# Optimization experiments

Measured on AMD Instinct MI355X. Metric: run time of the kernel, lower is better.

The kernel has to match this reference:

```python
import jax, jax.numpy as jnp
import numpy as np

N_HEADS = 16


def setup_inputs() -> dict:
    key = jax.random.key(0)
    ks = jax.random.split(key, 5)
    B, T, C = 4, 2048, 1024
    return {
        "x": jax.random.normal(ks[0], (B, T, C), dtype=jnp.float32),
        "W_qkv": jax.random.normal(ks[1], (C, 3 * C), dtype=jnp.float32) * 0.02,
        "b_qkv": jax.random.normal(ks[2], (3 * C,), dtype=jnp.float32) * 0.02,
        "W_proj": jax.random.normal(ks[3], (C, C), dtype=jnp.float32) * 0.02,
        "b_proj": jax.random.normal(ks[4], (C,), dtype=jnp.float32) * 0.02,
    }


def reference(x, W_qkv, b_qkv, W_proj, b_proj):
    B, T, C = x.shape
    H = N_HEADS
    hs = C // H
    # QKV projection. NOTE: original reshapes (B,T,3C) -> (B,T,H,3*hs) then
    # chunks last dim, so q/k/v are interleaved per-head slices of the output.
    qkv = x @ W_qkv + b_qkv                       # [B, T, 3C]
    qkv = qkv.reshape(B, T, H, 3 * hs).transpose(0, 2, 1, 3)  # [B, H, T, 3*hs]
    q, k, v = jnp.split(qkv, 3, axis=-1)          # each [B, H, T, hs]
    scale = 1.0 / (hs ** 0.5)
    scores = jnp.einsum("bhqd,bhkd->bhqk", q, k) * scale  # [B, H, T, T]
    causal = jnp.tril(jnp.ones((T, T), dtype=bool))
    scores = jnp.where(causal, scores, jnp.float32(-1e9))
    attn = jax.nn.softmax(scores, axis=-1)
    out = jnp.einsum("bhqk,bhkd->bhqd", attn, v)  # [B, H, T, hs]
    out = out.transpose(0, 2, 1, 3).reshape(B, T, C)
    return out @ W_proj + b_proj
```

## Files before the change

kernel.cpp:

```cpp
#include <hip/hip_runtime.h>

typedef unsigned short u16;
typedef unsigned int u32;
typedef __attribute__((ext_vector_type(8))) short short8;
typedef __attribute__((ext_vector_type(8))) unsigned short u16x8;
typedef __attribute__((ext_vector_type(4))) unsigned short u16x4;
typedef __attribute__((ext_vector_type(2))) unsigned int u32x2;
typedef __attribute__((ext_vector_type(4))) float f32x4;

__device__ __forceinline__ u16 f2bf(float f){
  u32 u = __builtin_bit_cast(u32, f);
  u32 r = u + 0x7FFFu + ((u >> 16) & 1u);
  return (u16)(r >> 16);
}
__device__ __forceinline__ float bf2f(u16 h){
  u32 u = ((u32)h) << 16;
  return __builtin_bit_cast(float, u);
}
__device__ __forceinline__ u32 cvtpk(float lo, float hi){
  u32 r;
  asm("v_cvt_pk_bf16_f32 %0, %1, %2" : "=v"(r) : "v"(lo), "v"(hi));
  return r;
}
__device__ __forceinline__ float fexp2(float x){
  float r;
  asm("v_exp_f32 %0, %1" : "=v"(r) : "v"(x));
  return r;
}

__device__ __forceinline__ void gld_lds16(const u16* g, u16* l){
  __builtin_amdgcn_global_load_lds(
      (const __attribute__((address_space(1))) u32*)g,
      (__attribute__((address_space(3))) u32*)l, 16, 0, 0);
}

#define MFMA(a,b,c) __builtin_amdgcn_mfma_f32_16x16x32_bf16((a),(b),(c),0,0,0)

__global__ __launch_bounds__(256) void k_prep(const float* __restrict__ x,
                                              u16* __restrict__ xb,
                                              const float* __restrict__ Wqkv,
                                              u16* __restrict__ wqkvT,
                                              const float* __restrict__ Wproj,
                                              u16* __restrict__ wprojT){
  __shared__ float tile[32][33];
  int bid = blockIdx.x, tid = threadIdx.x;
  if (bid < 4096){
    int i = bid*256 + tid;
    const float4 a = ((const float4*)x)[2*i];
    const float4 b = ((const float4*)x)[2*i+1];
    u16x8 o;
    o[0]=f2bf(a.x); o[1]=f2bf(a.y); o[2]=f2bf(a.z); o[3]=f2bf(a.w);
    o[4]=f2bf(b.x); o[5]=f2bf(b.y); o[6]=f2bf(b.z); o[7]=f2bf(b.w);
    ((u16x8*)xb)[i] = o;
    return;
  }
  const float* in; u16* out; int R, C, bx, by;
  if (bid < 7168){
    int b2 = bid - 4096;
    in = Wqkv; out = wqkvT; R = 1024; C = 3072;
    bx = b2 % 96; by = b2 / 96;
  } else {
    int b3 = bid - 7168;
    in = Wproj; out = wprojT; R = 1024; C = 1024;
    bx = b3 % 32; by = b3 / 32;
  }
  int c0 = bx*32, r0 = by*32;
  int tx = tid & 31, ty = tid >> 5;
  #pragma unroll
  for (int i=0;i<4;i++) tile[ty+8*i][tx] = in[(size_t)(r0+ty+8*i)*C + c0+tx];
  __syncthreads();
  #pragma unroll
  for (int i=0;i<4;i++) out[(size_t)(c0+ty+8*i)*R + r0+tx] = f2bf(tile[tx][ty+8*i]);
}

#define GS_A(T_, BUF) do{                                                      \
  size_t k0_ = (size_t)(T_)*64;                                                \
  _Pragma("unroll")                                                            \
  for (int l=0;l<2;l++){                                                       \
    int r_ = l*64 + (tid>>3);                                                  \
    gld_lds16(Ag + (size_t)(brow + r_)*1024 + k0_ + (((tid&7)^(r_&7))*8),      \
              &Alds[(BUF)*8192 + l*4096 + tid*8]);                             \
  }                                                                            \
}while(0)

#define GS_B(T_, BUF, H_) do{                                                  \
  size_t k0_ = (size_t)(T_)*64;                                                \
  _Pragma("unroll")                                                            \
  for (int l=0;l<2;l++){                                                       \
    int r_ = (H_)*128 + l*64 + (tid>>3);                                       \
    gld_lds16(Bg + (size_t)(bcol + r_)*1024 + k0_ + (((tid&7)^(r_&7))*8),      \
              &Blds[(BUF)*16384 + (H_)*8192 + l*4096 + tid*8]);                \
  }                                                                            \
}while(0)

#define RD_A(MQ, CUR) do{                                                      \
  _Pragma("unroll")                                                            \
  for (int m=0;m<2;m++)                                                        \
    _Pragma("unroll")                                                          \
    for (int k=0;k<2;k++){                                                     \
      int hr = wr*64 + (MQ)*32 + m*16 + lr16;                                  \
      af[(MQ)*2+m][k] = *(const short8*)&Alds[(CUR)*8192 + hr*64 + (((k*4+lg)^(hr&7))*8)]; \
    }                                                                          \
}while(0)

#define RD_B(NQ, CUR) do{                                                      \
  _Pragma("unroll")                                                            \
  for (int n=0;n<2;n++)                                                        \
    _Pragma("unroll")                                                          \
    for (int k=0;k<2;k++){                                                     \
      int hr = wc*64 + (NQ)*32 + n*16 + lr16;                                  \
      bfv[(NQ)*2+n][k] = *(const short8*)&Blds[(CUR)*16384 + hr*64 + (((k*4+lg)^(hr&7))*8)]; \
    }                                                                          \
}while(0)

#define MF8(MQ, NQ)                                                            \
  _Pragma("unroll")                                                            \
  for (int k=0;k<2;k++)                                                        \
    _Pragma("unroll")                                                          \
    for (int m=0;m<2;m++)                                                      \
      _Pragma("unroll")                                                        \
      for (int n=0;n<2;n++)                                                    \
        acc[(MQ)*2+m][(NQ)*2+n] = MFMA(af[(MQ)*2+m][k], bfv[(NQ)*2+n][k], acc[(MQ)*2+m][(NQ)*2+n]);

#define G_TILE(T_, CUR, PF) do{                                                \
  RD_A(0, CUR); RD_B(0, CUR);                                                  \
  if (PF) GS_A((T_)+1, (CUR)^1);                                               \
  __builtin_amdgcn_s_barrier();                                                \
  __builtin_amdgcn_s_setprio(1); MF8(0,0); __builtin_amdgcn_s_setprio(0);      \
  __builtin_amdgcn_s_barrier();                                                \
  RD_B(1, CUR);                                                                \
  if (PF) GS_B((T_)+1, (CUR)^1, 0);                                            \
  __builtin_amdgcn_s_barrier();                                                \
  __builtin_amdgcn_s_setprio(1); MF8(0,1); __builtin_amdgcn_s_setprio(0);      \
  __builtin_amdgcn_s_barrier();                                                \
  RD_A(1, CUR);                                                                \
  if (PF) GS_B((T_)+1, (CUR)^1, 1);                                            \
  __builtin_amdgcn_s_barrier();                                                \
  __builtin_amdgcn_s_setprio(1); MF8(1,1); __builtin_amdgcn_s_setprio(0);      \
  __builtin_amdgcn_s_barrier();                                                \
  __builtin_amdgcn_s_setprio(1); MF8(1,0); __builtin_amdgcn_s_setprio(0);      \
  asm volatile("s_waitcnt vmcnt(0)" ::: "memory");                             \
  __builtin_amdgcn_sched_barrier(0);                                           \
  __builtin_amdgcn_s_barrier();                                                \
}while(0)

template<int OUT_BF16>
__global__ __launch_bounds__(512, 2) void gemm_ph(const u16* __restrict__ Ag,
                                                  const u16* __restrict__ Bg,
                                                  const float* __restrict__ bias,
                                                  void* __restrict__ Cp, int N){
  extern __shared__ u16 lds[];
  u16* Alds = lds;
  u16* Blds = lds + 16384;
  int tid = threadIdx.x, lane = tid&63, wid = tid>>6;
  int wr = wid>>2, wc = wid&3;
  int lr16 = lane&15, lg = lane>>4;
  int nbx = gridDim.x;
  int nwg = nbx*gridDim.y;
  int lin = blockIdx.y*nbx + blockIdx.x;
  int cpx = nwg>>3;
  int swz = (lin&7)*cpx + (lin>>3);
  int bx = swz % nbx, by = swz / nbx;
  size_t brow = (size_t)by*128, bcol = (size_t)bx*256;
  f32x4 acc[4][4] = {};
  short8 af[4][2], bfv[4][2];

  GS_A(0, 0);
  GS_B(0, 0, 0);
  GS_B(0, 0, 1);
  __syncthreads();

  #pragma unroll 1
  for (int kt=0; kt<16; kt+=2){
    G_TILE(kt,   0, true);
    G_TILE(kt+1, 1, (kt+2<16));
  }

  #pragma unroll
  for (int ni=0;ni<4;ni++){
    size_t col = bcol + wc*64 + ni*16 + lr16;
    float bs = bias[col];
    #pragma unroll
    for (int mi=0;mi<4;mi++)
      #pragma unroll
      for (int j=0;j<4;j++){
        size_t row = brow + wr*64 + mi*16 + lg*4 + j;
        float v = acc[mi][ni][j] + bs;
        if (OUT_BF16) ((u16*)Cp)[row*(size_t)N + col] = f2bf(v);
        else          ((float*)Cp)[row*(size_t)N + col] = v;
      }
  }
}

#define ATTN_ITER(KB, CUR, PF) do{                                             \
  int kv0 = (KB)*64;                                                           \
  if (PF){                                                                     \
    int kv1 = kv0 + 64;                                                        \
    va[0] = *(const u16x4*)(qkv + (bt0 + kv1 + vr0    )*3072 + hq + 128 + vd0);\
    va[1] = *(const u16x4*)(qkv + (bt0 + kv1 + vr0 + 1)*3072 + hq + 128 + vd0);\
    gld_lds16(qkv + (bt0+kv1+kr)*3072 + hq + 64 + kcs, &Ks[(CUR)^1][tid*8]);   \
  }                                                                            \
  f32x4 st[4];                                                                 \
  __builtin_amdgcn_s_setprio(1);                                               \
  _Pragma("unroll")                                                            \
  for (int s=0;s<4;s++){                                                       \
    short8 kf0 = *(const short8*)&Ks[CUR][(s*16+lr16)*64 + ((lg  )^rx)*8];     \
    short8 kf1 = *(const short8*)&Ks[CUR][(s*16+lr16)*64 + ((4+lg)^rx)*8];     \
    f32x4 z = {0,0,0,0};                                                       \
    z = MFMA(kf0, qf[0], z);                                                   \
    z = MFMA(kf1, qf[1], z);                                                   \
    st[s] = z;                                                                 \
  }                                                                            \
  __builtin_amdgcn_s_setprio(0);                                               \
  if (kv0 >= qbase){                                                           \
    _Pragma("unroll")                                                          \
    for (int s=0;s<4;s++)                                                      \
      _Pragma("unroll")                                                        \
      for (int j=0;j<4;j++){                                                   \
        int kvg = kv0 + s*16 + lg*4 + j;                                       \
        if (kvg > qglob) st[s][j] = -1e30f;                                    \
      }                                                                        \
  }                                                                            \
  {                                                                            \
    u32 pw[8];                                                                 \
    _Pragma("unroll")                                                          \
    for (int s=0;s<4;s++){                                                     \
      float p0 = fexp2(st[s][0]), p1 = fexp2(st[s][1]);                        \
      float p2 = fexp2(st[s][2]), p3 = fexp2(st[s][3]);                        \
      pw[s*2+0] = cvtpk(p0,p1);                                                \
      pw[s*2+1] = cvtpk(p2,p3);                                                \
    }                                                                          \
    _Pragma("unroll")                                                          \
    for (int s=0;s<4;s++){                                                     \
      int cp = (s*2 + (lg>>1)) ^ rx;                                           \
      u32x2 w2; w2[0] = pw[s*2]; w2[1] = pw[s*2+1];                            \
      *(u32x2*)&Pl[wv][lr16*64 + cp*8 + (lg&1)*4] = w2;                        \
    }                                                                          \
  }                                                                            \
  if (PF){                                                                     \
    _Pragma("unroll")                                                          \
    for (int k=0;k<4;k++){                                                     \
      int d = vd0+k;                                                           \
      int c = (vr0>>3) ^ (d&7) ^ ((d>>3)&7);                                   \
      u32 w = (u32)va[0][k] | ((u32)va[1][k]<<16);                             \
      *(u32*)&Vt[(CUR)^1][d*64 + c*8 + (vr0&7)] = w;                           \
    }                                                                          \
  }                                                                            \
  __builtin_amdgcn_s_setprio(1);                                               \
  _Pragma("unroll")                                                            \
  for (int B=0;B<2;B++){                                                       \
    short8 pa = *(const short8*)&Pl[wv][lr16*64 + (((B<<2)+lg)^rx)*8];         \
    acc_l = MFMA(pa, onesf, acc_l);                                            \
    _Pragma("unroll")                                                          \
    for (int db=0;db<4;db++){                                                  \
      int d = db*16 + lr16;                                                    \
      short8 vf = *(const short8*)&Vt[CUR][d*64 + ((((B<<2)+lg)^(d&7))^((d>>3)&7))*8]; \
      O[db] = MFMA(pa, vf, O[db]);                                             \
    }                                                                          \
  }                                                                            \
  __builtin_amdgcn_s_setprio(0);                                               \
  __syncthreads();                                                             \
}while(0)

__global__ __launch_bounds__(512, 4) void k_attn(const u16* __restrict__ qkv,
                                                 u16* __restrict__ o, int T){
  __shared__ __align__(16) u16 Ks[2][64*64];
  __shared__ __align__(16) u16 Vt[2][64*64];
  __shared__ __align__(16) u16 Pl[8][16*64];
  int tid = threadIdx.x, lane = tid&63, wv = tid>>6;
  int bh = blockIdx.x;
  int b = bh>>4, h = bh&15;
  int hq = h*192;
  size_t bt0 = (size_t)b*T;
  int lr16 = lane&15, lg = lane>>4;
  int rx = lr16&7;
  int vr0 = (tid>>4)*2, vd0 = (tid&15)*4;
  int kr  = tid>>3;
  int kcs = ((tid&7) ^ (kr&7))*8;
  u16x4 va[2];
  const float QS = 0.18033688f;
  u16x8 ov;
  #pragma unroll
  for (int j=0;j<8;j++) ov[j] = 0x3F80;
  const short8 onesf = __builtin_bit_cast(short8, ov);

  #pragma unroll 1
  for (int half=0; half<2; ++half){
    int qt = half ? (int)blockIdx.y : 15 - (int)blockIdx.y;
    int qbase = qt*128;
    short8 qf[2];
    {
      const u16* qp = qkv + (bt0 + qbase + wv*16 + lr16)*3072 + hq + lg*8;
      #pragma unroll
      for (int t=0;t<2;t++){
        u16x8 v = *(const u16x8*)(qp + t*32);
        #pragma unroll
        for (int j=0;j<8;j++) v[j] = f2bf(bf2f(v[j])*QS);
        qf[t] = __builtin_bit_cast(short8, v);
      }
    }
    f32x4 O[4] = {};
    f32x4 acc_l = {0,0,0,0};
    int qglob = qbase + wv*16 + lr16;

    {
      va[0] = *(const u16x4*)(qkv + (bt0 + vr0    )*3072 + hq + 128 + vd0);
      va[1] = *(const u16x4*)(qkv + (bt0 + vr0 + 1)*3072 + hq + 128 + vd0);
      gld_lds16(qkv + (bt0+kr)*3072 + hq + 64 + kcs, &Ks[0][tid*8]);
      #pragma unroll
      for (int k=0;k<4;k++){
        int d = vd0+k;
        int c = (vr0>>3) ^ (d&7) ^ ((d>>3)&7);
        u32 w = (u32)va[0][k] | ((u32)va[1][k]<<16);
        *(u32*)&Vt[0][d*64 + c*8 + (vr0&7)] = w;
      }
    }
    __syncthreads();

    int nkv = 2*qt + 2;
    #pragma unroll 1
    for (int kb=0; kb<nkv; kb+=2){
      ATTN_ITER(kb,   0, true);
      ATTN_ITER(kb+1, 1, (kb+2<nkv));
    }
    {
      float lrow[4];
      #pragma unroll
      for (int j=0;j<4;j++) lrow[j] = __builtin_amdgcn_rcpf(acc_l[j]);
      #pragma unroll
      for (int db=0;db<4;db++)
        #pragma unroll
        for (int j=0;j<4;j++){
          size_t row = bt0 + qbase + wv*16 + lg*4 + j;
          o[row*1024 + h*64 + db*16 + lr16] = f2bf(O[db][j] * lrow[j]);
        }
    }
  }
}

extern "C" void kernel_launch(void* const* d_in, const int* in_sizes, int n_in,
                              void* d_out, int out_size, void* d_ws, size_t ws_size,
                              hipStream_t stream){
  (void)in_sizes; (void)n_in; (void)out_size; (void)ws_size;
  const float* x     = (const float*)d_in[0];
  const float* Wqkv  = (const float*)d_in[1];
  const float* bqkv  = (const float*)d_in[2];
  const float* Wproj = (const float*)d_in[3];
  const float* bproj = (const float*)d_in[4];
  float* out = (float*)d_out;
  const int T=2048, C=1024;
  char* ws = (char*)d_ws;
  u16* qkvb   = (u16*)(ws);
  u16* attnb  = (u16*)(ws + 50331648);
  u16* xb     = (u16*)(ws + 67108864);
  u16* wqkvT  = (u16*)(ws + 83886080);
  u16* wprojT = (u16*)(ws + 90177536);

  k_prep<<<8192, 256, 0, stream>>>(x, xb, Wqkv, wqkvT, Wproj, wprojT);
  gemm_ph<1><<<dim3(12,64), 512, 98304, stream>>>(xb, wqkvT, bqkv, qkvb, 3*C);
  k_attn<<<dim3(64,8), 512, 0, stream>>>(qkvb, attnb, T);
  gemm_ph<0><<<dim3(4,64), 512, 98304, stream>>>(attnb, wprojT, bproj, out, C);
}
```

Before: 158.9 us.

## Triple-buffer GEMM LDS tiles with prefetch two stages ahead

```diff
diff --git a/kernel.cpp b/kernel.cpp
--- a/kernel.cpp
+++ b/kernel.cpp
@@ -35,6 +35,8 @@
 }
 
 #define MFMA(a,b,c) __builtin_amdgcn_mfma_f32_16x16x32_bf16((a),(b),(c),0,0,0)
+#define STR2(x) #x
+#define VMWAIT(N) asm volatile("s_waitcnt vmcnt(" STR2(N) ")" ::: "memory")
 
 __global__ __launch_bounds__(256) void k_prep(const float* __restrict__ x,
                                               u16* __restrict__ xb,
@@ -122,36 +124,34 @@
       for (int n=0;n<2;n++)                                                    \
         acc[(MQ)*2+m][(NQ)*2+n] = MFMA(af[(MQ)*2+m][k], bfv[(NQ)*2+n][k], acc[(MQ)*2+m][(NQ)*2+n]);
 
-#define G_TILE(T_, CUR, PF) do{                                                \
+#define G_TILE(T_, CUR, PF, VMS) do{                                           \
   RD_A(0, CUR); RD_B(0, CUR);                                                  \
-  if (PF) GS_A((T_)+1, (CUR)^1);                                               \
   __builtin_amdgcn_s_barrier();                                                \
   __builtin_amdgcn_s_setprio(1); MF8(0,0); __builtin_amdgcn_s_setprio(0);      \
   __builtin_amdgcn_s_barrier();                                                \
   RD_B(1, CUR);                                                                \
-  if (PF) GS_B((T_)+1, (CUR)^1, 0);                                            \
   __builtin_amdgcn_s_barrier();                                                \
   __builtin_amdgcn_s_setprio(1); MF8(0,1); __builtin_amdgcn_s_setprio(0);      \
   __builtin_amdgcn_s_barrier();                                                \
   RD_A(1, CUR);                                                                \
-  if (PF) GS_B((T_)+1, (CUR)^1, 1);                                            \
   __builtin_amdgcn_s_barrier();                                                \
   __builtin_amdgcn_s_setprio(1); MF8(1,1); __builtin_amdgcn_s_setprio(0);      \
   __builtin_amdgcn_s_barrier();                                                \
   __builtin_amdgcn_s_setprio(1); MF8(1,0); __builtin_amdgcn_s_setprio(0);      \
-  asm volatile("s_waitcnt vmcnt(0)" ::: "memory");                             \
+  if (PF){ GS_A((T_)+3, CUR); GS_B((T_)+3, CUR, 0); GS_B((T_)+3, CUR, 1); }    \
+  VMWAIT(VMS);                                                                 \
   __builtin_amdgcn_sched_barrier(0);                                           \
   __builtin_amdgcn_s_barrier();                                                \
 }while(0)
 
 template<int OUT_BF16>
-__global__ __launch_bounds__(512, 2) void gemm_ph(const u16* __restrict__ Ag,
+__global__ __launch_bounds__(512, 1) void gemm_ph(const u16* __restrict__ Ag,
                                                   const u16* __restrict__ Bg,
                                                   const float* __restrict__ bias,
                                                   void* __restrict__ Cp, int N){
   extern __shared__ u16 lds[];
   u16* Alds = lds;
-  u16* Blds = lds + 16384;
+  u16* Blds = lds + 24576;
   int tid = threadIdx.x, lane = tid&63, wid = tid>>6;
   int wr = wid>>2, wc = wid&3;
   int lr16 = lane&15, lg = lane>>4;
@@ -165,16 +165,19 @@
   f32x4 acc[4][4] = {};
   short8 af[4][2], bfv[4][2];
 
-  GS_A(0, 0);
-  GS_B(0, 0, 0);
-  GS_B(0, 0, 1);
-  __syncthreads();
-
-  #pragma unroll 1
-  for (int kt=0; kt<16; kt+=2){
-    G_TILE(kt,   0, true);
-    G_TILE(kt+1, 1, (kt+2<16));
-  }
+  GS_A(0, 0); GS_B(0, 0, 0); GS_B(0, 0, 1);
+  GS_A(1, 1); GS_B(1, 1, 0); GS_B(1, 1, 1);
+  GS_A(2, 2); GS_B(2, 2, 0); GS_B(2, 2, 1);
+  VMWAIT(12);
+  __builtin_amdgcn_sched_barrier(0);
+  __builtin_amdgcn_s_barrier();
+
+  G_TILE( 0, 0, 1, 12); G_TILE( 1, 1, 1, 12); G_TILE( 2, 2, 1, 12);
+  G_TILE( 3, 0, 1, 12); G_TILE( 4, 1, 1, 12); G_TILE( 5, 2, 1, 12);
+  G_TILE( 6, 0, 1, 12); G_TILE( 7, 1, 1, 12); G_TILE( 8, 2, 1, 12);
+  G_TILE( 9, 0, 1, 12); G_TILE(10, 1, 1, 12); G_TILE(11, 2, 1, 12);
+  G_TILE(12, 0, 1, 12); G_TILE(13, 1, 0,  6); G_TILE(14, 2, 0,  0);
+  G_TILE(15, 0, 0,  0);
 
   #pragma unroll
   for (int ni=0;ni<4;ni++){
@@ -357,7 +360,7 @@
   u16* wprojT = (u16*)(ws + 90177536);
 
   k_prep<<<8192, 256, 0, stream>>>(x, xb, Wqkv, wqkvT, Wproj, wprojT);
-  gemm_ph<1><<<dim3(12,64), 512, 98304, stream>>>(xb, wqkvT, bqkv, qkvb, 3*C);
+  gemm_ph<1><<<dim3(12,64), 512, 147456, stream>>>(xb, wqkvT, bqkv, qkvb, 3*C);
   k_attn<<<dim3(64,8), 512, 0, stream>>>(qkvb, attnb, T);
-  gemm_ph<0><<<dim3(4,64), 512, 98304, stream>>>(attnb, wprojT, bproj, out, C);
-}
+  gemm_ph<0><<<dim3(4,64), 512, 147456, stream>>>(attnb, wprojT, bproj, out, C);
+}
```

After: 163.3 us. 1.03x slower.
